# Kernel tuning notes

Measured on AMD Instinct MI355X. Metric: run time of the kernel, lower is better.

Reference implementation:

```python
import jax, jax.numpy as jnp
import numpy as np

DELTA_INF = 1e10  # delta appended for the last sample, as in the torch code
EPS = 1e-10


def setup_inputs() -> dict:
    key = jax.random.key(0)
    k1, k2, k3 = jax.random.split(key, 3)
    N, S = 131072, 192
    ray_samples = jax.random.normal(k1, (N, S, 3), dtype=jnp.float32)
    densities = jax.random.normal(k2, (N, S, 1), dtype=jnp.float32)
    rgb = jax.random.uniform(k3, (N, S, 3), dtype=jnp.float32)
    background_color = jnp.ones((3,), dtype=jnp.float32)
    return {"ray_samples": ray_samples, "densities": densities, "rgb": rgb,
            "background_color": background_color}


def _render_weights(ray_samples, densities):
    # delta_i = ||x_{i+1} - x_i||, last delta = 1e10  -> [N, S, 1]
    diff = ray_samples[..., 1:, :] - ray_samples[..., :-1, :]
    delta = jnp.linalg.norm(diff, axis=-1, keepdims=True)
    delta = jnp.concatenate(
        [delta, jnp.full_like(delta[..., -1:, :], DELTA_INF)], axis=-2)
    alpha = 1.0 - jnp.exp(-jax.nn.relu(densities) * delta)
    # transmittance T_i = prod_{j<i} (1 - alpha_j + eps), exclusive cumprod
    trans = jnp.cumprod(
        jnp.concatenate(
            [jnp.ones_like(alpha[..., :1, :]), 1.0 - alpha + EPS], axis=-2),
        axis=-2)[..., :-1, :]
    weights = alpha * trans  # [N, S, 1]
    return weights


def reference(ray_samples, densities, rgb, background_color):
    weights = _render_weights(ray_samples, densities)
    rendered_rgb = jnp.sum(weights * rgb, axis=-2)           # [N, 3]
    accumulated_alpha = jnp.sum(weights, axis=-2)            # [N, 1]
    # composite with background: img + bg * (1 - acc)
    rendered_rgb = rendered_rgb + background_color * (1.0 - accumulated_alpha)
    return rendered_rgb, accumulated_alpha[..., 0], weights
```

## Files before the change

### kernel.cpp

```cpp
#include <hip/hip_runtime.h>

constexpr int NRAYS = 131072;
constexpr int S = 192;
constexpr float DELTA_INF_F = 1e10f;
constexpr float EPS_F = 1e-10f;

__global__ __launch_bounds__(256) void nerf_render_kernel(
    const float* __restrict__ ray_samples,
    const float* __restrict__ densities,
    const float* __restrict__ rgb,
    const float* __restrict__ bg,
    float* __restrict__ out_rgb,
    float* __restrict__ out_acc,
    float* __restrict__ out_w)
{
    const int lane = threadIdx.x & 63;
    const int ray  = (blockIdx.x << 2) + (threadIdx.x >> 6);

    const size_t rbase = (size_t)ray * S;

    const float* rs = ray_samples + rbase * 3 + lane * 9;
    float p[9];
#pragma unroll
    for (int j = 0; j < 9; ++j) p[j] = rs[j];

    float xn = __shfl_down(p[0], 1);
    float yn = __shfl_down(p[1], 1);
    float zn = __shfl_down(p[2], 1);

    float dx = p[3] - p[0], dy = p[4] - p[1], dz = p[5] - p[2];
    float d0 = sqrtf(dx*dx + dy*dy + dz*dz);
    dx = p[6] - p[3]; dy = p[7] - p[4]; dz = p[8] - p[5];
    float d1 = sqrtf(dx*dx + dy*dy + dz*dz);
    float d2 = DELTA_INF_F;
    if (lane < 63) {
        dx = xn - p[6]; dy = yn - p[7]; dz = zn - p[8];
        d2 = sqrtf(dx*dx + dy*dy + dz*dz);
    }

    const float* dn = densities + rbase + lane * 3;
    float e0 = expf(-fmaxf(dn[0], 0.0f) * d0);
    float e1 = expf(-fmaxf(dn[1], 0.0f) * d1);
    float e2 = expf(-fmaxf(dn[2], 0.0f) * d2);

    float a0 = 1.0f - e0, a1 = 1.0f - e1, a2 = 1.0f - e2;
    float t0 = (1.0f - a0) + EPS_F;
    float t1 = (1.0f - a1) + EPS_F;
    float t2 = (1.0f - a2) + EPS_F;

    float P = t0 * t1 * t2;
    float incl = P;
#pragma unroll
    for (int off = 1; off < 64; off <<= 1) {
        float t = __shfl_up(incl, off);
        if (lane >= off) incl *= t;
    }
    float pref = __shfl_up(incl, 1);
    if (lane == 0) pref = 1.0f;

    float w0 = a0 * pref;
    float w1 = a1 * pref * t0;
    float w2 = a2 * pref * t0 * t1;

    float* wout = out_w + rbase + lane * 3;
    wout[0] = w0; wout[1] = w1; wout[2] = w2;

    const float* cg = rgb + rbase * 3 + lane * 9;
    float cr = w0*cg[0] + w1*cg[3] + w2*cg[6];
    float cgrn = w0*cg[1] + w1*cg[4] + w2*cg[7];
    float cb = w0*cg[2] + w1*cg[5] + w2*cg[8];
    float acc = w0 + w1 + w2;

#pragma unroll
    for (int off = 32; off >= 1; off >>= 1) {
        cr   += __shfl_xor(cr, off);
        cgrn += __shfl_xor(cgrn, off);
        cb   += __shfl_xor(cb, off);
        acc  += __shfl_xor(acc, off);
    }

    if (lane == 0) {
        float om = 1.0f - acc;
        out_rgb[(size_t)ray*3 + 0] = cr   + bg[0] * om;
        out_rgb[(size_t)ray*3 + 1] = cgrn + bg[1] * om;
        out_rgb[(size_t)ray*3 + 2] = cb   + bg[2] * om;
        out_acc[ray] = acc;
    }
}

extern "C" void kernel_launch(void* const* d_in, const int* in_sizes, int n_in,
                              void* d_out, int out_size, void* d_ws, size_t ws_size,
                              hipStream_t stream) {
    const float* ray_samples = (const float*)d_in[0];
    const float* densities   = (const float*)d_in[1];
    const float* rgb         = (const float*)d_in[2];
    const float* bg          = (const float*)d_in[3];

    float* o = (float*)d_out;
    float* out_rgb = o;
    float* out_acc = o + (size_t)NRAYS * 3;
    float* out_w   = o + (size_t)NRAYS * 3 + NRAYS;

    dim3 grid(NRAYS / 4), block(256);
    hipLaunchKernelGGL(nerf_render_kernel, grid, block, 0, stream,
                       ray_samples, densities, rgb, bg, out_rgb, out_acc, out_w);
}
```

Measured before the change: 152.8 us.

## Stage per-ray data through LDS with coalesced float4 loads and stores

Loads positions, densities and rgb as contiguous float4 vectors per wavefront, stages positions and densities in shared memory, and writes weights back through an LDS buffer as coalesced float4 stores. The rgb dot product is restructured to use the float4 layout directly, with a lane-dependent channel rotation. This replaces the strided 9-float per-lane accesses that produced poorly coalesced memory traffic, at the cost of LDS usage, two block-wide barriers and more index arithmetic.

```diff
diff --git a/kernel.cpp b/kernel.cpp
--- a/kernel.cpp
+++ b/kernel.cpp
@@ -1,89 +1,133 @@
 #include <hip/hip_runtime.h>
 
 constexpr int NRAYS = 131072;
-constexpr int S = 192;
 constexpr float DELTA_INF_F = 1e10f;
 constexpr float EPS_F = 1e-10f;
 
 __global__ __launch_bounds__(256) void nerf_render_kernel(
-    const float* __restrict__ ray_samples,
-    const float* __restrict__ densities,
-    const float* __restrict__ rgb,
+    const float4* __restrict__ rsF4,
+    const float4* __restrict__ denF4,
+    const float4* __restrict__ rgbF4,
     const float* __restrict__ bg,
     float* __restrict__ out_rgb,
     float* __restrict__ out_acc,
-    float* __restrict__ out_w)
+    float4* __restrict__ out_wF4)
 {
+    __shared__ float pos[4][576];
+    __shared__ float den[4][192];
+    __shared__ float wbuf[4][192];
+
     const int lane = threadIdx.x & 63;
-    const int ray  = (blockIdx.x << 2) + (threadIdx.x >> 6);
+    const int w    = threadIdx.x >> 6;
+    const int ray  = (blockIdx.x << 2) + w;
 
-    const size_t rbase = (size_t)ray * S;
+    const float4* rg = rgbF4 + (size_t)ray * 144;
+    float4 c0 = rg[lane];
+    float4 c1 = rg[lane + 64];
+    float4 c2 = make_float4(0.f, 0.f, 0.f, 0.f);
+    if (lane < 16) c2 = rg[lane + 128];
 
-    const float* rs = ray_samples + rbase * 3 + lane * 9;
-    float p[9];
-#pragma unroll
-    for (int j = 0; j < 9; ++j) p[j] = rs[j];
+    const float4* rp = rsF4 + (size_t)ray * 144;
+    float4 p0 = rp[lane];
+    float4 p1 = rp[lane + 64];
+    float4 p2 = make_float4(0.f, 0.f, 0.f, 0.f);
+    if (lane < 16) p2 = rp[lane + 128];
 
-    float xn = __shfl_down(p[0], 1);
-    float yn = __shfl_down(p[1], 1);
-    float zn = __shfl_down(p[2], 1);
+    float4 dd = make_float4(0.f, 0.f, 0.f, 0.f);
+    if (lane < 48) dd = denF4[(size_t)ray * 48 + lane];
 
-    float dx = p[3] - p[0], dy = p[4] - p[1], dz = p[5] - p[2];
+    float4* pl = (float4*)&pos[w][0];
+    pl[lane]      = p0;
+    pl[lane + 64] = p1;
+    if (lane < 16) pl[lane + 128] = p2;
+    if (lane < 48) ((float4*)&den[w][0])[lane] = dd;
+
+    __syncthreads();
+
+    const int pb = 9 * lane;
+    float q0x = pos[w][pb+0], q0y = pos[w][pb+1], q0z = pos[w][pb+2];
+    float q1x = pos[w][pb+3], q1y = pos[w][pb+4], q1z = pos[w][pb+5];
+    float q2x = pos[w][pb+6], q2y = pos[w][pb+7], q2z = pos[w][pb+8];
+
+    float dx = q1x - q0x, dy = q1y - q0y, dz = q1z - q0z;
     float d0 = sqrtf(dx*dx + dy*dy + dz*dz);
-    dx = p[6] - p[3]; dy = p[7] - p[4]; dz = p[8] - p[5];
+    dx = q2x - q1x; dy = q2y - q1y; dz = q2z - q1z;
     float d1 = sqrtf(dx*dx + dy*dy + dz*dz);
     float d2 = DELTA_INF_F;
     if (lane < 63) {
-        dx = xn - p[6]; dy = yn - p[7]; dz = zn - p[8];
+        float nx = pos[w][pb+9], ny = pos[w][pb+10], nz = pos[w][pb+11];
+        dx = nx - q2x; dy = ny - q2y; dz = nz - q2z;
         d2 = sqrtf(dx*dx + dy*dy + dz*dz);
     }
 
-    const float* dn = densities + rbase + lane * 3;
-    float e0 = expf(-fmaxf(dn[0], 0.0f) * d0);
-    float e1 = expf(-fmaxf(dn[1], 0.0f) * d1);
-    float e2 = expf(-fmaxf(dn[2], 0.0f) * d2);
+    float s0 = den[w][3*lane+0], s1 = den[w][3*lane+1], s2 = den[w][3*lane+2];
+    float e0 = expf(-fmaxf(s0, 0.f) * d0);
+    float e1 = expf(-fmaxf(s1, 0.f) * d1);
+    float e2 = expf(-fmaxf(s2, 0.f) * d2);
 
-    float a0 = 1.0f - e0, a1 = 1.0f - e1, a2 = 1.0f - e2;
-    float t0 = (1.0f - a0) + EPS_F;
-    float t1 = (1.0f - a1) + EPS_F;
-    float t2 = (1.0f - a2) + EPS_F;
+    float a0 = 1.f - e0, a1 = 1.f - e1, a2 = 1.f - e2;
+    float t0 = (1.f - a0) + EPS_F;
+    float t1 = (1.f - a1) + EPS_F;
+    float t2 = (1.f - a2) + EPS_F;
 
-    float P = t0 * t1 * t2;
-    float incl = P;
+    float incl = t0 * t1 * t2;
 #pragma unroll
     for (int off = 1; off < 64; off <<= 1) {
         float t = __shfl_up(incl, off);
         if (lane >= off) incl *= t;
     }
     float pref = __shfl_up(incl, 1);
-    if (lane == 0) pref = 1.0f;
+    if (lane == 0) pref = 1.f;
 
     float w0 = a0 * pref;
     float w1 = a1 * pref * t0;
     float w2 = a2 * pref * t0 * t1;
+    float acc = w0 + w1 + w2;
 
-    float* wout = out_w + rbase + lane * 3;
-    wout[0] = w0; wout[1] = w1; wout[2] = w2;
+    wbuf[w][3*lane+0] = w0;
+    wbuf[w][3*lane+1] = w1;
+    wbuf[w][3*lane+2] = w2;
 
-    const float* cg = rgb + rbase * 3 + lane * 9;
-    float cr = w0*cg[0] + w1*cg[3] + w2*cg[6];
-    float cgrn = w0*cg[1] + w1*cg[4] + w2*cg[7];
-    float cb = w0*cg[2] + w1*cg[5] + w2*cg[8];
-    float acc = w0 + w1 + w2;
+    __syncthreads();
+
+    if (lane < 48)
+        out_wF4[(size_t)ray * 48 + lane] = ((const float4*)&wbuf[w][0])[lane];
+
+    float a_0 = 0.f, a_1 = 0.f, a_2 = 0.f;
+    {
+        const float* cv0 = &c0.x;
+        const float* cv1 = &c1.x;
+        const float* cv2 = &c2.x;
+#pragma unroll
+        for (int j = 0; j < 4; ++j) {
+            float m0 = cv0[j] * wbuf[w][lane + (lane + j) / 3];
+            if ((j + 0) % 3 == 0) a_0 += m0; else if ((j + 0) % 3 == 1) a_1 += m0; else a_2 += m0;
+            float m1 = cv1[j] * wbuf[w][lane + 85 + (lane + j + 1) / 3];
+            if ((j + 1) % 3 == 0) a_0 += m1; else if ((j + 1) % 3 == 1) a_1 += m1; else a_2 += m1;
+            if (lane < 16) {
+                float m2 = cv2[j] * wbuf[w][lane + 170 + (lane + j + 2) / 3];
+                if ((j + 2) % 3 == 0) a_0 += m2; else if ((j + 2) % 3 == 1) a_1 += m2; else a_2 += m2;
+            }
+        }
+    }
+    const int b = lane % 3;
+    float cr = (b == 0) ? a_0 : ((b == 1) ? a_2 : a_1);
+    float cg = (b == 0) ? a_1 : ((b == 1) ? a_0 : a_2);
+    float cb = (b == 0) ? a_2 : ((b == 1) ? a_1 : a_0);
 
 #pragma unroll
     for (int off = 32; off >= 1; off >>= 1) {
-        cr   += __shfl_xor(cr, off);
-        cgrn += __shfl_xor(cgrn, off);
-        cb   += __shfl_xor(cb, off);
-        acc  += __shfl_xor(acc, off);
+        cr  += __shfl_xor(cr, off);
+        cg  += __shfl_xor(cg, off);
+        cb  += __shfl_xor(cb, off);
+        acc += __shfl_xor(acc, off);
     }
 
     if (lane == 0) {
-        float om = 1.0f - acc;
-        out_rgb[(size_t)ray*3 + 0] = cr   + bg[0] * om;
-        out_rgb[(size_t)ray*3 + 1] = cgrn + bg[1] * om;
-        out_rgb[(size_t)ray*3 + 2] = cb   + bg[2] * om;
+        float om = 1.f - acc;
+        out_rgb[(size_t)ray*3 + 0] = cr + bg[0] * om;
+        out_rgb[(size_t)ray*3 + 1] = cg + bg[1] * om;
+        out_rgb[(size_t)ray*3 + 2] = cb + bg[2] * om;
         out_acc[ray] = acc;
     }
 }
@@ -91,17 +135,17 @@
 extern "C" void kernel_launch(void* const* d_in, const int* in_sizes, int n_in,
                               void* d_out, int out_size, void* d_ws, size_t ws_size,
                               hipStream_t stream) {
-    const float* ray_samples = (const float*)d_in[0];
-    const float* densities   = (const float*)d_in[1];
-    const float* rgb         = (const float*)d_in[2];
-    const float* bg          = (const float*)d_in[3];
+    const float4* rsF4  = (const float4*)d_in[0];
+    const float4* denF4 = (const float4*)d_in[1];
+    const float4* rgbF4 = (const float4*)d_in[2];
+    const float*  bg    = (const float*)d_in[3];
 
     float* o = (float*)d_out;
-    float* out_rgb = o;
-    float* out_acc = o + (size_t)NRAYS * 3;
-    float* out_w   = o + (size_t)NRAYS * 3 + NRAYS;
+    float*  out_rgb = o;
+    float*  out_acc = o + (size_t)NRAYS * 3;
+    float4* out_wF4 = (float4*)(o + (size_t)NRAYS * 4);
 
     dim3 grid(NRAYS / 4), block(256);
     hipLaunchKernelGGL(nerf_render_kernel, grid, block, 0, stream,
-                       ray_samples, densities, rgb, bg, out_rgb, out_acc, out_w);
+                       rsF4, denF4, rgbF4, bg, out_rgb, out_acc, out_wF4);
 }
```

After: 159.9 us. +4.6%, slower.
